# Kernel tuning notes

Measured on AMD Instinct MI355X. Metric: run time of the kernel, lower is better.

The kernel has to match this reference:

```python
import jax, jax.numpy as jnp
import numpy as np

N = 50000      # nodes
E = 800000     # edges (before self loops)
IN = 256       # in_channels
HID = 64       # hidden_channels
HEADS = 2
NEG_SLOPE = 0.2
BN_EPS = 1e-5


def setup_inputs() -> dict:
    key = jax.random.key(0)
    ks = jax.random.split(key, 16)
    def g(i, shape, scale=0.05):
        return jax.random.normal(ks[i], shape, dtype=jnp.float32) * scale
    return {
        "x": jax.random.normal(ks[0], (N, IN), dtype=jnp.float32),
        "edge_index": jax.random.randint(ks[1], (2, E), 0, N, dtype=jnp.int64).astype(jnp.int32),
        # conv1 (GATv2, heads=2, concat)
        "W1l": g(2, (IN, HEADS * HID)), "b1l": jnp.zeros(HEADS * HID, jnp.float32),
        "W1r": g(3, (IN, HEADS * HID)), "b1r": jnp.zeros(HEADS * HID, jnp.float32),
        "att1": g(4, (HEADS, HID)), "bias1": jnp.zeros(HEADS * HID, jnp.float32),
        "bn1_g": jnp.ones(HEADS * HID, jnp.float32), "bn1_b": jnp.zeros(HEADS * HID, jnp.float32),
        "bn1_m": jnp.zeros(HEADS * HID, jnp.float32), "bn1_v": jnp.ones(HEADS * HID, jnp.float32),
        # conv2 (GATv2, heads=1)
        "W2l": g(5, (HEADS * HID, HID)), "b2l": jnp.zeros(HID, jnp.float32),
        "W2r": g(6, (HEADS * HID, HID)), "b2r": jnp.zeros(HID, jnp.float32),
        "att2": g(7, (1, HID)), "bias2": jnp.zeros(HID, jnp.float32),
        "bn2_g": jnp.ones(HID, jnp.float32), "bn2_b": jnp.zeros(HID, jnp.float32),
        "bn2_m": jnp.zeros(HID, jnp.float32), "bn2_v": jnp.ones(HID, jnp.float32),
        # classifier
        "Wc": g(8, (HID, 1)), "bc": jnp.zeros(1, jnp.float32),
    }


def _gatv2(x, src, dst, Wl, bl, Wr, br, att, bias, heads, ch, n):
    # GATv2: e_ij = att . leaky_relu(Wl x_j + Wr x_i); segment softmax over dst; out_i = sum alpha_ij Wl x_j
    xl = (x @ Wl + bl).reshape(n, heads, ch)  # source transform [N,H,C]
    xr = (x @ Wr + br).reshape(n, heads, ch)  # target transform [N,H,C]
    e = jax.nn.leaky_relu(xl[src] + xr[dst], NEG_SLOPE)        # [E,H,C]
    logits = jnp.einsum('ehc,hc->eh', e, att)                  # [E,H]
    m = jax.ops.segment_max(logits, dst, num_segments=n)       # [N,H]
    p = jnp.exp(logits - m[dst])
    s = jax.ops.segment_sum(p, dst, num_segments=n)            # [N,H]
    alpha = p / s[dst]                                         # [E,H]
    out = jax.ops.segment_sum(alpha[:, :, None] * xl[src], dst, num_segments=n)  # [N,H,C]
    return out.reshape(n, heads * ch) + bias


def _bn(x, g, b, m, v):
    return (x - m) * jax.lax.rsqrt(v + BN_EPS) * g + b


def reference(x, edge_index, W1l, b1l, W1r, b1r, att1, bias1,
              bn1_g, bn1_b, bn1_m, bn1_v,
              W2l, b2l, W2r, b2r, att2, bias2,
              bn2_g, bn2_b, bn2_m, bn2_v, Wc, bc):
    n = x.shape[0]
    loop = jnp.arange(n, dtype=edge_index.dtype)  # add_self_loops=True
    src = jnp.concatenate([edge_index[0], loop])
    dst = jnp.concatenate([edge_index[1], loop])
    h = _gatv2(x, src, dst, W1l, b1l, W1r, b1r, att1, bias1, HEADS, HID, n)
    h = jax.nn.elu(_bn(h, bn1_g, bn1_b, bn1_m, bn1_v))
    h = _gatv2(h, src, dst, W2l, b2l, W2r, b2r, att2, bias2, 1, HID, n)
    h = jax.nn.elu(_bn(h, bn2_g, bn2_b, bn2_m, bn2_v))
    return jax.nn.sigmoid(h @ Wc + bc)
```

## Files before the change

kernel.cpp:

```cpp
#include <hip/hip_runtime.h>
#include <hip/hip_bf16.h>
#include <cstddef>

#define NN 50000
#define EE 800000
#define TE 850000
#define INC 256
#define C1 128
#define C2 64
#define NCHUNK 49

#define NB_COUNT 3321
#define NB_CAST  3125
#define NB_P1    256
#define NB_P2    128
#define NB_K1    (NB_COUNT + NB_CAST + NB_P1 + NB_P2)
#define NB_GEMM1 782
#define NB_K2    (NB_GEMM1 + NB_COUNT)

#define LOG2E 1.44269504088896340736f

typedef unsigned short ushort_t;
typedef short bf16x8 __attribute__((ext_vector_type(8)));
typedef float f32x4 __attribute__((ext_vector_type(4)));

__device__ inline ushort_t bf16r(float f) {
    unsigned u = __float_as_uint(f);
    unsigned r = (u + 0x7fffu + ((u >> 16) & 1u)) >> 16;
    return (ushort_t)r;
}
#define LOF(u) (__uint_as_float((u) << 16))
#define HIF(u) (__uint_as_float((u) & 0xffff0000u))
#define ELU(t) ((t) > 0.f ? (t) : (__expf(t) - 1.f))


__global__ void k_scan1(const int* __restrict__ deg, int* __restrict__ incl,
                        int* __restrict__ totals) {
    __shared__ int lds[1024];
    int t = threadIdx.x;
    int i = blockIdx.x * 1024 + t;
    int v = (i < NN) ? deg[i] : 0;
    lds[t] = v;
    __syncthreads();
    for (int off = 1; off < 1024; off <<= 1) {
        int add = (t >= off) ? lds[t - off] : 0;
        __syncthreads();
        lds[t] += add;
        __syncthreads();
    }
    if (i < NN) incl[i] = lds[t];
    if (t == 1023) totals[blockIdx.x] = lds[t];
}

__global__ void k_scan3(const int* __restrict__ incl, const int* __restrict__ deg,
                        const int* __restrict__ totals, int* __restrict__ rowstart) {
    int i = blockIdx.x * blockDim.x + threadIdx.x;
    if (i == 0) rowstart[NN] = TE;
    if (i >= NN) return;
    int chunk = blockIdx.x >> 2;
    int coff = 0;
    for (int c = 0; c < chunk; c++) coff += totals[c];
    rowstart[i] = incl[i] - deg[i] + coff;
}


__global__ __launch_bounds__(256) void k_stage1(
    const int* __restrict__ ei, int* __restrict__ deg, int* __restrict__ rank,
    const float* __restrict__ x, ushort_t* __restrict__ xb,
    const float* __restrict__ W1l, const float* __restrict__ W1r,
    const float* __restrict__ b1l, const float* __restrict__ b1r,
    ushort_t* __restrict__ Wt1, float* __restrict__ biasf1,
    const float* __restrict__ W2l, const float* __restrict__ W2r,
    const float* __restrict__ b2l, const float* __restrict__ b2r,
    ushort_t* __restrict__ Wt2, float* __restrict__ biasf2) {
    int b = blockIdx.x;
    int tid = threadIdx.x;
    if (b < NB_COUNT) {
        int e = b * 256 + tid;
        if (e < TE) {
            int dst = (e < EE) ? ei[EE + e] : (e - EE);
            rank[e] = atomicAdd(&deg[dst], 1);
        }
    } else if (b < NB_COUNT + NB_CAST) {
        int i0 = (b - NB_COUNT) * 1024 + tid;
        float4 a[4];
#pragma unroll
        for (int k = 0; k < 4; k++) a[k] = ((const float4*)x)[i0 + k * 256];
#pragma unroll
        for (int k = 0; k < 4; k++) {
            ushort4 o;
            o.x = bf16r(a[k].x); o.y = bf16r(a[k].y);
            o.z = bf16r(a[k].z); o.w = bf16r(a[k].w);
            ((ushort4*)xb)[i0 + k * 256] = o;
        }
    } else if (b < NB_COUNT + NB_CAST + NB_P1) {
        int n = b - NB_COUNT - NB_CAST;
        int k = tid;
        const float* W = (n < 128) ? W1l : W1r;
        int c = (n < 128) ? n : n - 128;
        Wt1[(size_t)n * 256 + k] = bf16r(W[(size_t)k * 128 + c]);
        if (n == 0) biasf1[k] = (k < 128) ? b1l[k] : b1r[k - 128];
    } else {
        int n = b - NB_COUNT - NB_CAST - NB_P1;
        int k = tid;
        if (k < 128) {
            const float* W = (n < 64) ? W2l : W2r;
            int c = (n < 64) ? n : n - 64;
            Wt2[(size_t)n * 128 + k] = bf16r(W[(size_t)k * 64 + c]);
            if (n == 0) biasf2[k] = (k < 64) ? b2l[k] : b2r[k - 64];
        }
    }
}


template <int K, int NCOL>
__device__ inline void gemm_body(const ushort_t* __restrict__ A,
                                 const ushort_t* __restrict__ Bt,
                                 const float* __restrict__ bias,
                                 ushort_t* __restrict__ C, int M,
                                 int bm, int bn, ushort_t* As, ushort_t* Bs) {
    int tid = threadIdx.x;
    int w = tid >> 6, l = tid & 63;
    int wm = (w & 1) * 64, wn = (w >> 1) * 64;
    int lm = l & 15, half = l >> 4;

    f32x4 zero = {0.f, 0.f, 0.f, 0.f};
    f32x4 acc[4][4];
#pragma unroll
    for (int a = 0; a < 4; a++)
#pragma unroll
        for (int b = 0; b < 4; b++) acc[a][b] = zero;

    for (int k0 = 0; k0 < K; k0 += 32) {
#pragma unroll
        for (int q = 0; q < 2; q++) {
            int seg = q * 256 + tid;
            int m = seg >> 2;
            int ko = (seg & 3) * 8;
            *(float4*)&As[m * 40 + ko] = *(const float4*)&A[(size_t)(bm + m) * K + k0 + ko];
            *(float4*)&Bs[m * 40 + ko] = *(const float4*)&Bt[(size_t)(bn + m) * K + k0 + ko];
        }
        __syncthreads();
        bf16x8 af[4], bfr[4];
#pragma unroll
        for (int mi = 0; mi < 4; mi++)
            af[mi] = *(const bf16x8*)&As[(wm + mi * 16 + lm) * 40 + half * 8];
#pragma unroll
        for (int ni = 0; ni < 4; ni++)
            bfr[ni] = *(const bf16x8*)&Bs[(wn + ni * 16 + lm) * 40 + half * 8];
#pragma unroll
        for (int mi = 0; mi < 4; mi++)
#pragma unroll
            for (int ni = 0; ni < 4; ni++)
                acc[mi][ni] = __builtin_amdgcn_mfma_f32_16x16x32_bf16(
                    af[mi], bfr[ni], acc[mi][ni], 0, 0, 0);
        __syncthreads();
    }
#pragma unroll
    for (int ni = 0; ni < 4; ni++) {
        int col = bn + wn + ni * 16 + lm;
        float bv = bias[col];
#pragma unroll
        for (int mi = 0; mi < 4; mi++) {
            int rbase = bm + wm + mi * 16 + half * 4;
#pragma unroll
            for (int r = 0; r < 4; r++) {
                int row = rbase + r;
                if (row < M) C[(size_t)row * NCOL + col] = bf16r(acc[mi][ni][r] + bv);
            }
        }
    }
}


__global__ __launch_bounds__(256) void k_gemm1_scatter(
    const ushort_t* __restrict__ A, const ushort_t* __restrict__ Bt,
    const float* __restrict__ bias, ushort_t* __restrict__ C,
    const int* __restrict__ ei, const int* __restrict__ rank,
    const int* __restrict__ rowstart, int* __restrict__ ssrc) {
    __shared__ __align__(16) ushort_t As[128 * 40];
    __shared__ __align__(16) ushort_t Bs[128 * 40];
    int b = blockIdx.x;
    if (b < NB_GEMM1) {
        int bm = (b >> 1) * 128;
        int bn = (b & 1) * 128;
        gemm_body<256, 256>(A, Bt, bias, C, NN, bm, bn, As, Bs);
    } else {
        int e = (b - NB_GEMM1) * 256 + threadIdx.x;
        if (e < TE) {
            int s, d;
            if (e < EE) { s = ei[e]; d = ei[EE + e]; }
            else        { s = e - EE; d = s; }
            ssrc[rowstart[d] + rank[e]] = s;
        }
    }
}

__global__ __launch_bounds__(256) void k_gemm2(
    const ushort_t* __restrict__ A, const ushort_t* __restrict__ Bt,
    const float* __restrict__ bias, ushort_t* __restrict__ C) {
    __shared__ __align__(16) ushort_t As[128 * 40];
    __shared__ __align__(16) ushort_t Bs[128 * 40];
    int bm = blockIdx.x * 128;
    gemm_body<128, 128>(A, Bt, bias, C, NN, bm, 0, As, Bs);
}


__global__ __launch_bounds__(256) void k_fused1(
    const ushort_t* __restrict__ xlr, const int* __restrict__ rowstart,
    const int* __restrict__ ssrc, const float* __restrict__ att,
    const float* __restrict__ bias,
    const float* __restrict__ g, const float* __restrict__ b,
    const float* __restrict__ m, const float* __restrict__ v,
    ushort_t* __restrict__ out) {
    int lane = threadIdx.x & 63;
    int i = blockIdx.x * 4 + (threadIdx.x >> 6);
    if (i >= NN) return;
    int hw = lane >> 5;
    int c2 = lane & 31;
    uint2 xru = *(const uint2*)&xlr[(size_t)i * 256 + 128 + 4 * c2];
    float xr0 = LOF(xru.x), xr1 = HIF(xru.x), xr2 = LOF(xru.y), xr3 = HIF(xru.y);
    float4 at = *(const float4*)&att[4 * c2];
    float4 a6 = make_float4(at.x * (0.6f * LOG2E), at.y * (0.6f * LOG2E),
                            at.z * (0.6f * LOG2E), at.w * (0.6f * LOG2E));
    float4 a4 = make_float4(at.x * (0.4f * LOG2E), at.y * (0.4f * LOG2E),
                            at.z * (0.4f * LOG2E), at.w * (0.4f * LOG2E));
    int row = rowstart[i], end = rowstart[i + 1];
    float a0 = 0.f, a1 = 0.f, a2 = 0.f, a3 = 0.f, s = 0.f;
    int j = row;
    for (; j + 8 <= end; j += 8) {
        int src[4];
        uint2 u[4];
#pragma unroll
        for (int k = 0; k < 4; k++) src[k] = ssrc[j + 2 * k + hw];
#pragma unroll
        for (int k = 0; k < 4; k++)
            u[k] = *(const uint2*)&xlr[(size_t)src[k] * 256 + 4 * c2];
        float d[4], f0[4], f1[4], f2[4], f3[4];
#pragma unroll
        for (int k = 0; k < 4; k++) {
            f0[k] = LOF(u[k].x); f1[k] = HIF(u[k].x);
            f2[k] = LOF(u[k].y); f3[k] = HIF(u[k].y);
            float t0 = f0[k] + xr0, t1 = f1[k] + xr1;
            float t2 = f2[k] + xr2, t3 = f3[k] + xr3;
            float dd = fmaf(a6.x, t0, a4.x * fabsf(t0));
            dd = fmaf(a6.y, t1, fmaf(a4.y, fabsf(t1), dd));
            dd = fmaf(a6.z, t2, fmaf(a4.z, fabsf(t2), dd));
            dd = fmaf(a6.w, t3, fmaf(a4.w, fabsf(t3), dd));
            d[k] = dd;
        }
#pragma unroll
        for (int o = 1; o <= 8; o <<= 1) {
#pragma unroll
            for (int k = 0; k < 4; k++) d[k] += __shfl_xor(d[k], o, 64);
        }
#pragma unroll
        for (int k = 0; k < 4; k++) {
            float p = exp2f(d[k]);
            a0 += p * f0[k]; a1 += p * f1[k];
            a2 += p * f2[k]; a3 += p * f3[k];
            s += p;
        }
    }
    for (; j < end; j += 2) {
        int je = j + hw;
        bool valid = je < end;
        int src = valid ? ssrc[je] : i;
        uint2 uu = *(const uint2*)&xlr[(size_t)src * 256 + 4 * c2];
        float f0 = LOF(uu.x), f1 = HIF(uu.x), f2 = LOF(uu.y), f3 = HIF(uu.y);
        float t0 = f0 + xr0, t1 = f1 + xr1, t2 = f2 + xr2, t3 = f3 + xr3;
        float dd = fmaf(a6.x, t0, a4.x * fabsf(t0));
        dd = fmaf(a6.y, t1, fmaf(a4.y, fabsf(t1), dd));
        dd = fmaf(a6.z, t2, fmaf(a4.z, fabsf(t2), dd));
        dd = fmaf(a6.w, t3, fmaf(a4.w, fabsf(t3), dd));
        dd += __shfl_xor(dd, 1, 64);
        dd += __shfl_xor(dd, 2, 64);
        dd += __shfl_xor(dd, 4, 64);
        dd += __shfl_xor(dd, 8, 64);
        float p = valid ? exp2f(dd) : 0.f;
        a0 += p * f0; a1 += p * f1; a2 += p * f2; a3 += p * f3;
        s += p;
    }
    a0 += __shfl_xor(a0, 32, 64);
    a1 += __shfl_xor(a1, 32, 64);
    a2 += __shfl_xor(a2, 32, 64);
    a3 += __shfl_xor(a3, 32, 64);
    s  += __shfl_xor(s, 32, 64);
    if (hw == 0) {
        float inv = 1.f / s;
        float4 bb = *(const float4*)&bias[4 * c2];
        float4 mm = *(const float4*)&m[4 * c2];
        float4 vv = *(const float4*)&v[4 * c2];
        float4 gg = *(const float4*)&g[4 * c2];
        float4 b2 = *(const float4*)&b[4 * c2];
        float o0 = a0 * inv + bb.x, o1 = a1 * inv + bb.y;
        float o2 = a2 * inv + bb.z, o3 = a3 * inv + bb.w;
        o0 = (o0 - mm.x) * rsqrtf(vv.x + 1e-5f) * gg.x + b2.x;
        o1 = (o1 - mm.y) * rsqrtf(vv.y + 1e-5f) * gg.y + b2.y;
        o2 = (o2 - mm.z) * rsqrtf(vv.z + 1e-5f) * gg.z + b2.z;
        o3 = (o3 - mm.w) * rsqrtf(vv.w + 1e-5f) * gg.w + b2.w;
        o0 = ELU(o0); o1 = ELU(o1); o2 = ELU(o2); o3 = ELU(o3);
        uint2 wp;
        wp.x = (unsigned)bf16r(o0) | ((unsigned)bf16r(o1) << 16);
        wp.y = (unsigned)bf16r(o2) | ((unsigned)bf16r(o3) << 16);
        *(uint2*)&out[(size_t)i * C1 + 4 * c2] = wp;
    }
}

__global__ __launch_bounds__(256) void k_fused2(
    const ushort_t* __restrict__ xlr, const int* __restrict__ rowstart,
    const int* __restrict__ ssrc, const float* __restrict__ att,
    const float* __restrict__ bias,
    const float* __restrict__ g, const float* __restrict__ b,
    const float* __restrict__ m, const float* __restrict__ v,
    const float* __restrict__ Wc, const float* __restrict__ bc,
    float* __restrict__ out) {
    int lane = threadIdx.x & 63;
    int i = blockIdx.x * 4 + (threadIdx.x >> 6);
    if (i >= NN) return;
    int qw = lane >> 4;
    int c4 = lane & 15;
    uint2 xru = *(const uint2*)&xlr[(size_t)i * 128 + 64 + 4 * c4];
    float xr0 = LOF(xru.x), xr1 = HIF(xru.x), xr2 = LOF(xru.y), xr3 = HIF(xru.y);
    float4 at = *(const float4*)&att[4 * c4];
    float4 a6 = make_float4(at.x * (0.6f * LOG2E), at.y * (0.6f * LOG2E),
                            at.z * (0.6f * LOG2E), at.w * (0.6f * LOG2E));
    float4 a4 = make_float4(at.x * (0.4f * LOG2E), at.y * (0.4f * LOG2E),
                            at.z * (0.4f * LOG2E), at.w * (0.4f * LOG2E));
    int row = rowstart[i], end = rowstart[i + 1];
    float a0 = 0.f, a1 = 0.f, a2 = 0.f, a3 = 0.f, s = 0.f;
    int j = row;
    for (; j + 16 <= end; j += 16) {
        int src[4];
        uint2 u[4];
#pragma unroll
        for (int k = 0; k < 4; k++) src[k] = ssrc[j + 4 * k + qw];
#pragma unroll
        for (int k = 0; k < 4; k++)
            u[k] = *(const uint2*)&xlr[(size_t)src[k] * 128 + 4 * c4];
        float d[4], f0[4], f1[4], f2[4], f3[4];
#pragma unroll
        for (int k = 0; k < 4; k++) {
            f0[k] = LOF(u[k].x); f1[k] = HIF(u[k].x);
            f2[k] = LOF(u[k].y); f3[k] = HIF(u[k].y);
            float t0 = f0[k] + xr0, t1 = f1[k] + xr1;
            float t2 = f2[k] + xr2, t3 = f3[k] + xr3;
            float dd = fmaf(a6.x, t0, a4.x * fabsf(t0));
            dd = fmaf(a6.y, t1, fmaf(a4.y, fabsf(t1), dd));
            dd = fmaf(a6.z, t2, fmaf(a4.z, fabsf(t2), dd));
            dd = fmaf(a6.w, t3, fmaf(a4.w, fabsf(t3), dd));
            d[k] = dd;
        }
#pragma unroll
        for (int o = 1; o <= 8; o <<= 1) {
#pragma unroll
            for (int k = 0; k < 4; k++) d[k] += __shfl_xor(d[k], o, 64);
        }
#pragma unroll
        for (int k = 0; k < 4; k++) {
            float p = exp2f(d[k]);
            a0 += p * f0[k]; a1 += p * f1[k];
            a2 += p * f2[k]; a3 += p * f3[k];
            s += p;
        }
    }
    if (j + 8 <= end) {
        int src[2];
        uint2 u[2];
#pragma unroll
        for (int k = 0; k < 2; k++) src[k] = ssrc[j + 4 * k + qw];
#pragma unroll
        for (int k = 0; k < 2; k++)
            u[k] = *(const uint2*)&xlr[(size_t)src[k] * 128 + 4 * c4];
#pragma unroll
        for (int k = 0; k < 2; k++) {
            float f0 = LOF(u[k].x), f1 = HIF(u[k].x), f2 = LOF(u[k].y), f3 = HIF(u[k].y);
            float t0 = f0 + xr0, t1 = f1 + xr1, t2 = f2 + xr2, t3 = f3 + xr3;
            float dd = fmaf(a6.x, t0, a4.x * fabsf(t0));
            dd = fmaf(a6.y, t1, fmaf(a4.y, fabsf(t1), dd));
            dd = fmaf(a6.z, t2, fmaf(a4.z, fabsf(t2), dd));
            dd = fmaf(a6.w, t3, fmaf(a4.w, fabsf(t3), dd));
            dd += __shfl_xor(dd, 1, 64);
            dd += __shfl_xor(dd, 2, 64);
            dd += __shfl_xor(dd, 4, 64);
            dd += __shfl_xor(dd, 8, 64);
            float p = exp2f(dd);
            a0 += p * f0; a1 += p * f1; a2 += p * f2; a3 += p * f3;
            s += p;
        }
        j += 8;
    }
    for (; j < end; j += 4) {
        int je = j + qw;
        bool valid = je < end;
        int src = valid ? ssrc[je] : i;
        uint2 uu = *(const uint2*)&xlr[(size_t)src * 128 + 4 * c4];
        float f0 = LOF(uu.x), f1 = HIF(uu.x), f2 = LOF(uu.y), f3 = HIF(uu.y);
        float t0 = f0 + xr0, t1 = f1 + xr1, t2 = f2 + xr2, t3 = f3 + xr3;
        float dd = fmaf(a6.x, t0, a4.x * fabsf(t0));
        dd = fmaf(a6.y, t1, fmaf(a4.y, fabsf(t1), dd));
        dd = fmaf(a6.z, t2, fmaf(a4.z, fabsf(t2), dd));
        dd = fmaf(a6.w, t3, fmaf(a4.w, fabsf(t3), dd));
        dd += __shfl_xor(dd, 1, 64);
        dd += __shfl_xor(dd, 2, 64);
        dd += __shfl_xor(dd, 4, 64);
        dd += __shfl_xor(dd, 8, 64);
        float p = valid ? exp2f(dd) : 0.f;
        a0 += p * f0; a1 += p * f1; a2 += p * f2; a3 += p * f3;
        s += p;
    }
#pragma unroll
    for (int o = 16; o <= 32; o <<= 1) {
        a0 += __shfl_xor(a0, o, 64);
        a1 += __shfl_xor(a1, o, 64);
        a2 += __shfl_xor(a2, o, 64);
        a3 += __shfl_xor(a3, o, 64);
        s  += __shfl_xor(s, o, 64);
    }
    float inv = 1.f / s;
    float4 bb = *(const float4*)&bias[4 * c4];
    float4 mm = *(const float4*)&m[4 * c4];
    float4 vv = *(const float4*)&v[4 * c4];
    float4 gg = *(const float4*)&g[4 * c4];
    float4 b2 = *(const float4*)&b[4 * c4];
    float o0 = a0 * inv + bb.x, o1 = a1 * inv + bb.y;
    float o2 = a2 * inv + bb.z, o3 = a3 * inv + bb.w;
    o0 = (o0 - mm.x) * rsqrtf(vv.x + 1e-5f) * gg.x + b2.x;
    o1 = (o1 - mm.y) * rsqrtf(vv.y + 1e-5f) * gg.y + b2.y;
    o2 = (o2 - mm.z) * rsqrtf(vv.z + 1e-5f) * gg.z + b2.z;
    o3 = (o3 - mm.w) * rsqrtf(vv.w + 1e-5f) * gg.w + b2.w;
    o0 = ELU(o0); o1 = ELU(o1); o2 = ELU(o2); o3 = ELU(o3);
    float4 wc = *(const float4*)&Wc[4 * c4];
    float z = o0 * wc.x + o1 * wc.y + o2 * wc.z + o3 * wc.w;
    z += __shfl_xor(z, 1, 64);
    z += __shfl_xor(z, 2, 64);
    z += __shfl_xor(z, 4, 64);
    z += __shfl_xor(z, 8, 64);
    if (lane == 0) out[i] = 1.f / (1.f + __expf(-(z + bc[0])));
}


extern "C" void kernel_launch(void* const* d_in, const int* in_sizes, int n_in,
                              void* d_out, int out_size, void* d_ws, size_t ws_size,
                              hipStream_t stream) {
    const float* x    = (const float*)d_in[0];
    const int*   ei   = (const int*)d_in[1];
    const float* W1l  = (const float*)d_in[2];
    const float* b1l  = (const float*)d_in[3];
    const float* W1r  = (const float*)d_in[4];
    const float* b1r  = (const float*)d_in[5];
    const float* att1 = (const float*)d_in[6];
    const float* bias1= (const float*)d_in[7];
    const float* bn1g = (const float*)d_in[8];
    const float* bn1b = (const float*)d_in[9];
    const float* bn1m = (const float*)d_in[10];
    const float* bn1v = (const float*)d_in[11];
    const float* W2l  = (const float*)d_in[12];
    const float* b2l  = (const float*)d_in[13];
    const float* W2r  = (const float*)d_in[14];
    const float* b2r  = (const float*)d_in[15];
    const float* att2 = (const float*)d_in[16];
    const float* bias2= (const float*)d_in[17];
    const float* bn2g = (const float*)d_in[18];
    const float* bn2b = (const float*)d_in[19];
    const float* bn2m = (const float*)d_in[20];
    const float* bn2v = (const float*)d_in[21];
    const float* Wc   = (const float*)d_in[22];
    const float* bc   = (const float*)d_in[23];
    float* out = (float*)d_out;

    char* ws = (char*)d_ws;
    size_t off = 0;
    auto alloc = [&](size_t bytes) {
        size_t o = off;
        off += (bytes + 255) & ~(size_t)255;
        return o;
    };
    ushort_t* xb    = (ushort_t*)(ws + alloc((size_t)(NN + 128) * 256 * 2));
    ushort_t* xlr1  = (ushort_t*)(ws + alloc((size_t)NN * 256 * 2));
    ushort_t* h1b   = (ushort_t*)(ws + alloc((size_t)(NN + 128) * 128 * 2));
    ushort_t* Wt1   = (ushort_t*)(ws + alloc((size_t)256 * 256 * 2));
    float*    biasf1= (float*)(ws + alloc(256 * 4));
    ushort_t* Wt2   = (ushort_t*)(ws + alloc((size_t)128 * 128 * 2));
    float*    biasf2= (float*)(ws + alloc(128 * 4));
    int* deg      = (int*)(ws + alloc((size_t)NN * 4));
    int* incl     = (int*)(ws + alloc((size_t)NN * 4));
    int* rowstart = (int*)(ws + alloc((size_t)(NN + 1) * 4));
    int* totals   = (int*)(ws + alloc(64 * 4));
    int* rank     = (int*)(ws + alloc((size_t)TE * 4));
    int* ssrc     = (int*)(ws + alloc((size_t)TE * 4));
    ushort_t* xlr2 = xlr1;

    hipMemsetAsync(deg, 0, (size_t)NN * 4, stream);

    k_stage1<<<NB_K1, 256, 0, stream>>>(ei, deg, rank, x, xb,
                                        W1l, W1r, b1l, b1r, Wt1, biasf1,
                                        W2l, W2r, b2l, b2r, Wt2, biasf2);

    k_scan1<<<NCHUNK, 1024, 0, stream>>>(deg, incl, totals);
    k_scan3<<<(NN + 255) / 256, 256, 0, stream>>>(incl, deg, totals, rowstart);

    k_gemm1_scatter<<<NB_K2, 256, 0, stream>>>(xb, Wt1, biasf1, xlr1,
                                               ei, rank, rowstart, ssrc);

    k_fused1<<<(NN + 3) / 4, 256, 0, stream>>>(xlr1, rowstart, ssrc, att1, bias1,
                                               bn1g, bn1b, bn1m, bn1v, h1b);

    k_gemm2<<<(NN + 127) / 128, 256, 0, stream>>>(h1b, Wt2, biasf2, xlr2);
    k_fused2<<<(NN + 3) / 4, 256, 0, stream>>>(xlr2, rowstart, ssrc, att2, bias2,
                                               bn2g, bn2b, bn2m, bn2v, Wc, bc, out);
}
```

Measured before the change: 294.4 us.

## Replicate degree counters eight ways to spread atomic contention in CSR build

Degree counting now uses eight replicated counter arrays, chosen by block index, so the per-destination atomics are spread across more addresses. The scan kernels sum the replicas, compute per-replica offsets for the scatter, and replace the serial per-thread loop over chunk totals with a wave reduction. This targets atomic serialization in the edge-count pass, at the cost of more memset, scan reads and writes, and an extra offset array. The renaming of locals in the fused kernel is cosmetic.

```diff
diff --git a/kernel.cpp b/kernel.cpp
--- a/kernel.cpp
+++ b/kernel.cpp
@@ -9,6 +9,7 @@
 #define C1 128
 #define C2 64
 #define NCHUNK 49
+#define NREP 8
 
 #define NB_COUNT 3321
 #define NB_CAST  3125
@@ -34,12 +35,17 @@
 #define ELU(t) ((t) > 0.f ? (t) : (__expf(t) - 1.f))
 
 
-__global__ void k_scan1(const int* __restrict__ deg, int* __restrict__ incl,
-                        int* __restrict__ totals) {
+__global__ void k_scan1(const int* __restrict__ deg8, int* __restrict__ degt,
+                        int* __restrict__ incl, int* __restrict__ totals) {
     __shared__ int lds[1024];
     int t = threadIdx.x;
     int i = blockIdx.x * 1024 + t;
-    int v = (i < NN) ? deg[i] : 0;
+    int v = 0;
+    if (i < NN) {
+#pragma unroll
+        for (int r = 0; r < NREP; r++) v += deg8[r * NN + i];
+        degt[i] = v;
+    }
     lds[t] = v;
     __syncthreads();
     for (int off = 1; off < 1024; off <<= 1) {
@@ -52,20 +58,33 @@
     if (t == 1023) totals[blockIdx.x] = lds[t];
 }
 
-__global__ void k_scan3(const int* __restrict__ incl, const int* __restrict__ deg,
-                        const int* __restrict__ totals, int* __restrict__ rowstart) {
+__global__ void k_scan3(const int* __restrict__ incl, const int* __restrict__ degt,
+                        const int* __restrict__ deg8, const int* __restrict__ totals,
+                        int* __restrict__ rowstart, int* __restrict__ off8) {
+    __shared__ int sOff;
+    int chunk = blockIdx.x >> 2;
+    if (threadIdx.x < 64) {
+        int t = (threadIdx.x < chunk) ? totals[threadIdx.x] : 0;
+#pragma unroll
+        for (int o = 1; o <= 32; o <<= 1) t += __shfl_xor(t, o, 64);
+        if (threadIdx.x == 0) sOff = t;
+    }
+    __syncthreads();
     int i = blockIdx.x * blockDim.x + threadIdx.x;
     if (i == 0) rowstart[NN] = TE;
     if (i >= NN) return;
-    int chunk = blockIdx.x >> 2;
-    int coff = 0;
-    for (int c = 0; c < chunk; c++) coff += totals[c];
-    rowstart[i] = incl[i] - deg[i] + coff;
+    int base = incl[i] - degt[i] + sOff;
+    rowstart[i] = base;
+#pragma unroll
+    for (int r = 0; r < NREP; r++) {
+        off8[r * NN + i] = base;
+        base += deg8[r * NN + i];
+    }
 }
 
 
 __global__ __launch_bounds__(256) void k_stage1(
-    const int* __restrict__ ei, int* __restrict__ deg, int* __restrict__ rank,
+    const int* __restrict__ ei, int* __restrict__ deg8, int* __restrict__ rank,
     const float* __restrict__ x, ushort_t* __restrict__ xb,
     const float* __restrict__ W1l, const float* __restrict__ W1r,
     const float* __restrict__ b1l, const float* __restrict__ b1r,
@@ -79,7 +98,7 @@
         int e = b * 256 + tid;
         if (e < TE) {
             int dst = (e < EE) ? ei[EE + e] : (e - EE);
-            rank[e] = atomicAdd(&deg[dst], 1);
+            rank[e] = atomicAdd(&deg8[(b & 7) * NN + dst], 1);
         }
     } else if (b < NB_COUNT + NB_CAST) {
         int i0 = (b - NB_COUNT) * 1024 + tid;
@@ -177,7 +196,7 @@
     const ushort_t* __restrict__ A, const ushort_t* __restrict__ Bt,
     const float* __restrict__ bias, ushort_t* __restrict__ C,
     const int* __restrict__ ei, const int* __restrict__ rank,
-    const int* __restrict__ rowstart, int* __restrict__ ssrc) {
+    const int* __restrict__ off8, int* __restrict__ ssrc) {
     __shared__ __align__(16) ushort_t As[128 * 40];
     __shared__ __align__(16) ushort_t Bs[128 * 40];
     int b = blockIdx.x;
@@ -191,7 +210,8 @@
             int s, d;
             if (e < EE) { s = ei[e]; d = ei[EE + e]; }
             else        { s = e - EE; d = s; }
-            ssrc[rowstart[d] + rank[e]] = s;
+            int r = (e >> 8) & 7;
+            ssrc[off8[r * NN + d] + rank[e]] = s;
         }
     }
 }
@@ -365,16 +385,16 @@
         }
     }
     if (j + 8 <= end) {
-        int src[2];
-        uint2 u[2];
-#pragma unroll
-        for (int k = 0; k < 2; k++) src[k] = ssrc[j + 4 * k + qw];
+        int src2[2];
+        uint2 u2[2];
+#pragma unroll
+        for (int k = 0; k < 2; k++) src2[k] = ssrc[j + 4 * k + qw];
 #pragma unroll
         for (int k = 0; k < 2; k++)
-            u[k] = *(const uint2*)&xlr[(size_t)src[k] * 128 + 4 * c4];
+            u2[k] = *(const uint2*)&xlr[(size_t)src2[k] * 128 + 4 * c4];
 #pragma unroll
         for (int k = 0; k < 2; k++) {
-            float f0 = LOF(u[k].x), f1 = HIF(u[k].x), f2 = LOF(u[k].y), f3 = HIF(u[k].y);
+            float f0 = LOF(u2[k].x), f1 = HIF(u2[k].x), f2 = LOF(u2[k].y), f3 = HIF(u2[k].y);
             float t0 = f0 + xr0, t1 = f1 + xr1, t2 = f2 + xr2, t3 = f3 + xr3;
             float dd = fmaf(a6.x, t0, a4.x * fabsf(t0));
             dd = fmaf(a6.y, t1, fmaf(a4.y, fabsf(t1), dd));
@@ -483,25 +503,28 @@
     float*    biasf1= (float*)(ws + alloc(256 * 4));
     ushort_t* Wt2   = (ushort_t*)(ws + alloc((size_t)128 * 128 * 2));
     float*    biasf2= (float*)(ws + alloc(128 * 4));
-    int* deg      = (int*)(ws + alloc((size_t)NN * 4));
+    int* deg8     = (int*)(ws + alloc((size_t)NREP * NN * 4));
+    int* degt     = (int*)(ws + alloc((size_t)NN * 4));
     int* incl     = (int*)(ws + alloc((size_t)NN * 4));
     int* rowstart = (int*)(ws + alloc((size_t)(NN + 1) * 4));
+    int* off8     = (int*)(ws + alloc((size_t)NREP * NN * 4));
     int* totals   = (int*)(ws + alloc(64 * 4));
     int* rank     = (int*)(ws + alloc((size_t)TE * 4));
     int* ssrc     = (int*)(ws + alloc((size_t)TE * 4));
     ushort_t* xlr2 = xlr1;
 
-    hipMemsetAsync(deg, 0, (size_t)NN * 4, stream);
-
-    k_stage1<<<NB_K1, 256, 0, stream>>>(ei, deg, rank, x, xb,
+    hipMemsetAsync(deg8, 0, (size_t)NREP * NN * 4, stream);
+
+    k_stage1<<<NB_K1, 256, 0, stream>>>(ei, deg8, rank, x, xb,
                                         W1l, W1r, b1l, b1r, Wt1, biasf1,
                                         W2l, W2r, b2l, b2r, Wt2, biasf2);
 
-    k_scan1<<<NCHUNK, 1024, 0, stream>>>(deg, incl, totals);
-    k_scan3<<<(NN + 255) / 256, 256, 0, stream>>>(incl, deg, totals, rowstart);
+    k_scan1<<<NCHUNK, 1024, 0, stream>>>(deg8, degt, incl, totals);
+    k_scan3<<<(NN + 255) / 256, 256, 0, stream>>>(incl, degt, deg8, totals,
+                                                  rowstart, off8);
 
     k_gemm1_scatter<<<NB_K2, 256, 0, stream>>>(xb, Wt1, biasf1, xlr1,
-                                               ei, rank, rowstart, ssrc);
+                                               ei, rank, off8, ssrc);
 
     k_fused1<<<(NN + 3) / 4, 256, 0, stream>>>(xlr1, rowstart, ssrc, att1, bias1,
                                                bn1g, bn1b, bn1m, bn1v, h1b);
```

Result: no change. 292.3 us (median of 2 runs) (-0.7%).
